# Kernel tuning notes

Hardware: AMD Instinct MI355X
Metric: run time of the kernel (lower is better)

Reference implementation:

```python
import jax, jax.numpy as jnp
import numpy as np

N, E, F0, HEADS, B, OUT = 100000, 1600000, 128, 4, 64, 32
CHANNELS = [16, 8, 4, 2]
NEG_SLOPE = 0.2


def setup_inputs() -> dict:
    key = jax.random.key(0)
    ks = jax.random.split(key, 40)
    inp = {}
    inp['x'] = jax.random.normal(ks[0], (N, F0), dtype=jnp.float32)
    inp['edge_index'] = jax.random.randint(ks[1], (2, E), 0, N, dtype=jnp.int64)
    inp['batch'] = jnp.sort(jax.random.randint(ks[2], (N,), 0, B, dtype=jnp.int64))
    # GATConv params per layer: W [in, heads*out], att_src/att_dst [heads, out], bias [heads*out]
    in_dim = F0
    ki = 3
    for li, oc in enumerate(CHANNELS, start=1):
        scale = 1.0 / np.sqrt(in_dim)
        inp[f'W{li}'] = jax.random.normal(ks[ki], (in_dim, HEADS * oc), dtype=jnp.float32) * scale
        inp[f'a_src{li}'] = jax.random.normal(ks[ki + 1], (HEADS, oc), dtype=jnp.float32) * 0.1
        inp[f'a_dst{li}'] = jax.random.normal(ks[ki + 2], (HEADS, oc), dtype=jnp.float32) * 0.1
        inp[f'b{li}'] = jnp.zeros((HEADS * oc,), dtype=jnp.float32)
        ki += 3
        in_dim = HEADS * oc
    inp['W_fc'] = jax.random.normal(ks[ki], (2 * HEADS, OUT), dtype=jnp.float32) * (1.0 / np.sqrt(2 * HEADS))
    inp['b_fc'] = jnp.zeros((OUT,), dtype=jnp.float32)
    return inp


def gat_layer(x, src, dst, W, a_src, a_dst, b, oc):
    n = x.shape[0]
    h = (x @ W).reshape(n, HEADS, oc)                    # [N, H, C]
    al_s = jnp.einsum('nhc,hc->nh', h, a_src)            # [N, H]
    al_d = jnp.einsum('nhc,hc->nh', h, a_dst)
    e = jax.nn.leaky_relu(al_s[src] + al_d[dst], NEG_SLOPE)  # [E, H]
    # segment softmax over incoming edges per destination node
    m = jax.ops.segment_max(e, dst, num_segments=n)
    m = jnp.where(jnp.isfinite(m), m, 0.0)
    ex = jnp.exp(e - m[dst])
    s = jax.ops.segment_sum(ex, dst, num_segments=n)
    alpha = ex / (s[dst] + 1e-16)                        # [E, H]
    out = jax.ops.segment_sum(h[src] * alpha[:, :, None], dst, num_segments=n)
    return out.reshape(n, HEADS * oc) + b


def reference(x, edge_index, batch, W1, a_src1, a_dst1, b1, W2, a_src2, a_dst2, b2,
              W3, a_src3, a_dst3, b3, W4, a_src4, a_dst4, b4, W_fc, b_fc):
    n = x.shape[0]
    loops = jnp.arange(n, dtype=edge_index.dtype)
    src = jnp.concatenate([edge_index[0], loops])   # PyG GATConv adds self-loops
    dst = jnp.concatenate([edge_index[1], loops])
    params = [(W1, a_src1, a_dst1, b1), (W2, a_src2, a_dst2, b2),
              (W3, a_src3, a_dst3, b3), (W4, a_src4, a_dst4, b4)]
    h = x
    for (W, a_s, a_d, b), oc in zip(params, CHANNELS):
        h = jax.nn.relu(gat_layer(h, src, dst, W, a_s, a_d, b, oc))
        # dropout(0.3) is identity at inference
    # global mean pool over graphs in the batch
    sums = jax.ops.segment_sum(h, batch, num_segments=B)
    cnt = jax.ops.segment_sum(jnp.ones((n,), h.dtype), batch, num_segments=B)
    pooled = sums / jnp.maximum(cnt, 1.0)[:, None]
    return pooled @ W_fc + b_fc
```

## Files before the change

kernel.cpp:

```cpp
#include <hip/hip_runtime.h>
#include <hip/hip_bf16.h>

#define NNODES 100000
#define NEDGES 1600000
#define NHEADS 4
#define NGRAPH 64
#define NOUTF  32
#define BSH    9
#define NBUK   ((NNODES + 511) >> 9)
#define BPAD   16
#define BCAP   9216
#define CGRID  512
#define G1GRID ((NNODES + 63) / 64)

__device__ __forceinline__ unsigned short f2bf(float f) {
    union { float f; unsigned u; } v;
    v.f = f;
    unsigned r = v.u + 0x7FFF + ((v.u >> 16) & 1);
    return (unsigned short)(r >> 16);
}
__device__ __forceinline__ float bflo(unsigned u) {
    union { unsigned u; float f; } v;
    v.u = u << 16;
    return v.f;
}
__device__ __forceinline__ float bfhi(unsigned u) {
    union { unsigned u; float f; } v;
    v.u = u & 0xFFFF0000u;
    return v.f;
}

__device__ __forceinline__ bool ei_is_int64(const int* __restrict__ ei) {
    int acc = 0;
    #pragma unroll
    for (int i = 0; i < 32; i++) acc |= ei[2 * i + 1];
    return acc == 0;
}

__device__ __forceinline__ void fma4(float4& a, float s, const float4& b) {
    a.x += s * b.x;
    a.y += s * b.y;
    a.z += s * b.z;
    a.w += s * b.w;
}

__global__ __launch_bounds__(256) void gat_coarse_gemm1_kernel(
        const int* __restrict__ ei, const int* __restrict__ bt,
        int* __restrict__ bkcur, int* __restrict__ packed, int* __restrict__ bat,
        const float* __restrict__ x, const float* __restrict__ W1,
        const float* __restrict__ as1, const float* __restrict__ ad1,
        unsigned short* __restrict__ h1, float* __restrict__ al_s,
        float* __restrict__ al_d, int ne, int n) {
    __shared__ float smem[64 * 64 + 64 * 132];
    const int tid = threadIdx.x;
    if (blockIdx.x < CGRID) {
        int* hist = (int*)smem;
        int* base = hist + NBUK;
        for (int i = tid; i < NBUK; i += 256) hist[i] = 0;
        __syncthreads();
        bool wide = ei_is_int64(ei);
        int chunk = (ne + CGRID - 1) / CGRID;
        int e0 = blockIdx.x * chunk;
        int e1 = min(e0 + chunk, ne);
        for (int i = e0 + tid; i < e1; i += 256) {
            int d = wide ? ei[2 * (ne + i)] : ei[ne + i];
            atomicAdd(&hist[d >> BSH], 1);
        }
        __syncthreads();
        for (int i = tid; i < NBUK; i += 256)
            base[i] = hist[i] ? atomicAdd(&bkcur[i * BPAD], hist[i]) : 0;
        __syncthreads();
        for (int i = tid; i < NBUK; i += 256) hist[i] = 0;
        __syncthreads();
        for (int i = e0 + tid; i < e1; i += 256) {
            int s = wide ? ei[2 * i] : ei[i];
            int d = wide ? ei[2 * (ne + i)] : ei[ne + i];
            int bk = d >> BSH;
            int pos = base[bk] + atomicAdd(&hist[bk], 1);
            if (pos < BCAP) packed[bk * BCAP + pos] = s | ((d & 511) << 17);
        }
        int gid = blockIdx.x * 256 + tid;
        for (int i = gid; i < n; i += CGRID * 256) bat[i] = wide ? bt[2 * i] : bt[i];
    } else {
        constexpr int DIN = 128, DOUT = 64, KTILE = 64;
        constexpr int OG = DOUT / 4;
        constexpr int NPB = 64;
        constexpr int S = DIN + 4;
        constexpr int C = DOUT / NHEADS;
        float* Wl = smem;
        float* xs = smem + KTILE * DOUT;
        const int base = (blockIdx.x - CGRID) * NPB;
        constexpr int KC = DIN / 4;
        for (int i = tid; i < NPB * KC; i += 256) {
            int nn = i / KC, kc = i - nn * KC;
            int nd = base + nn;
            float4 v = (nd < n) ? ((const float4*)x)[(size_t)nd * KC + kc]
                                : make_float4(0.f, 0.f, 0.f, 0.f);
            *(float4*)&xs[nn * S + kc * 4] = v;
        }
        const int og = tid % OG;
        const int ng = tid / OG;
        const int n0 = ng * 4;
        float4 acc[4] = {};
        for (int kt = 0; kt < DIN; kt += KTILE) {
            __syncthreads();
            for (int i = tid; i < KTILE * OG; i += 256)
                ((float4*)Wl)[i] = ((const float4*)W1)[kt * OG + i];
            __syncthreads();
            #pragma unroll 2
            for (int k = 0; k < KTILE; k += 4) {
                float4 wv[4], xv[4];
                #pragma unroll
                for (int j = 0; j < 4; j++)
                    wv[j] = *(const float4*)&Wl[(k + j) * DOUT + og * 4];
                #pragma unroll
                for (int r = 0; r < 4; r++)
                    xv[r] = *(const float4*)&xs[(n0 + r) * S + kt + k];
                #pragma unroll
                for (int r = 0; r < 4; r++) {
                    fma4(acc[r], xv[r].x, wv[0]);
                    fma4(acc[r], xv[r].y, wv[1]);
                    fma4(acc[r], xv[r].z, wv[2]);
                    fma4(acc[r], xv[r].w, wv[3]);
                }
            }
        }
        float4 asv = ((const float4*)as1)[og];
        float4 adv = ((const float4*)ad1)[og];
        #pragma unroll
        for (int r = 0; r < 4; r++) {
            int node = base + n0 + r;
            bool ok = node < n;
            if (ok) {
                ushort4 o;
                o.x = f2bf(acc[r].x);
                o.y = f2bf(acc[r].y);
                o.z = f2bf(acc[r].z);
                o.w = f2bf(acc[r].w);
                ((ushort4*)h1)[(size_t)node * OG + og] = o;
            }
            float ps = acc[r].x * asv.x + acc[r].y * asv.y + acc[r].z * asv.z + acc[r].w * asv.w;
            float pd = acc[r].x * adv.x + acc[r].y * adv.y + acc[r].z * adv.z + acc[r].w * adv.w;
            #pragma unroll
            for (int off = 1; off < C / 4; off <<= 1) {
                ps += __shfl_xor(ps, off);
                pd += __shfl_xor(pd, off);
            }
            if (ok && (og % (C / 4)) == 0) {
                int hh = og / (C / 4);
                al_s[node * NHEADS + hh] = ps;
                al_d[node * NHEADS + hh] = pd;
            }
        }
    }
}

__global__ __launch_bounds__(1024) void gat_fine_kernel(
        const int* __restrict__ packed, const int* __restrict__ bkcur,
        int* __restrict__ row_ptr, int* __restrict__ col, int n) {
    __shared__ int bscan[256];
    __shared__ int dg[512];
    __shared__ int excl[512];
    __shared__ int partial[256];
    __shared__ int cur[512];
    int b = blockIdx.x;
    int tid = threadIdx.x;
    if (tid < 256) bscan[tid] = (tid < NBUK) ? bkcur[tid * BPAD] : 0;
    if (tid < 512) dg[tid] = 0;
    __syncthreads();
    for (int off = 1; off < 256; off <<= 1) {
        int u = (tid < 256 && tid >= off) ? bscan[tid - off] : 0;
        __syncthreads();
        if (tid < 256) bscan[tid] += u;
        __syncthreads();
    }
    int cntb = bkcur[b * BPAD];
    int csr0 = bscan[b] - cntb;
    int pbeg = b * BCAP;
    int pend = pbeg + cntb;
    for (int t = pbeg + tid; t < pend; t += 1024)
        atomicAdd(&dg[packed[t] >> 17], 1);
    __syncthreads();
    int a0 = 0, a1 = 0, s = 0;
    if (tid < 256) {
        a0 = dg[2 * tid];
        a1 = dg[2 * tid + 1];
        s = a0 + a1;
        partial[tid] = s;
    }
    __syncthreads();
    for (int off = 1; off < 256; off <<= 1) {
        int u = (tid < 256 && tid >= off) ? partial[tid - off] : 0;
        __syncthreads();
        if (tid < 256) partial[tid] += u;
        __syncthreads();
    }
    if (tid < 256) {
        int ebase = partial[tid] - s;
        excl[2 * tid] = ebase;
        excl[2 * tid + 1] = ebase + a0;
        cur[2 * tid] = ebase;
        cur[2 * tid + 1] = ebase + a0;
    }
    __syncthreads();
    int node0 = b << BSH;
    if (tid < 512) {
        int nd = node0 + tid;
        if (nd < n) row_ptr[nd] = csr0 + excl[tid];
    }
    if (b == NBUK - 1 && tid == 0) row_ptr[n] = bscan[NBUK - 1];
    for (int t = pbeg + tid; t < pend; t += 1024) {
        int v = packed[t];
        int pos = atomicAdd(&cur[v >> 17], 1);
        col[csr0 + pos] = v & 0x1FFFF;
    }
}

template<int DIN, int DOUT, int KTILE, bool BF16OUT>
__global__ __launch_bounds__(256) void gat_gemm_attn_kernel(
        const float* __restrict__ in, const float* __restrict__ W,
        const float* __restrict__ a_src, const float* __restrict__ a_dst,
        void* __restrict__ hout, float* __restrict__ al_s, float* __restrict__ al_d, int n) {
    constexpr int OG = DOUT / 4;
    constexpr int NPB = 1024 / OG;
    constexpr int S = DIN + 4;
    constexpr int C = DOUT / NHEADS;
    __shared__ float Wl[KTILE * DOUT];
    __shared__ float xs[NPB * S];
    const int tid = threadIdx.x;
    const int base = blockIdx.x * NPB;
    constexpr int KC = DIN / 4;
    for (int i = tid; i < NPB * KC; i += 256) {
        int nn = i / KC, kc = i - nn * KC;
        int nd = base + nn;
        float4 v = (nd < n) ? ((const float4*)in)[(size_t)nd * KC + kc]
                            : make_float4(0.f, 0.f, 0.f, 0.f);
        *(float4*)&xs[nn * S + kc * 4] = v;
    }
    const int og = tid % OG;
    const int ng = tid / OG;
    const int n0 = ng * 4;
    float4 acc[4] = {};
    for (int kt = 0; kt < DIN; kt += KTILE) {
        __syncthreads();
        for (int i = tid; i < KTILE * OG; i += 256)
            ((float4*)Wl)[i] = ((const float4*)W)[kt * OG + i];
        __syncthreads();
        #pragma unroll 2
        for (int k = 0; k < KTILE; k += 4) {
            float4 wv[4], xv[4];
            #pragma unroll
            for (int j = 0; j < 4; j++)
                wv[j] = *(const float4*)&Wl[(k + j) * DOUT + og * 4];
            #pragma unroll
            for (int r = 0; r < 4; r++)
                xv[r] = *(const float4*)&xs[(n0 + r) * S + kt + k];
            #pragma unroll
            for (int r = 0; r < 4; r++) {
                fma4(acc[r], xv[r].x, wv[0]);
                fma4(acc[r], xv[r].y, wv[1]);
                fma4(acc[r], xv[r].z, wv[2]);
                fma4(acc[r], xv[r].w, wv[3]);
            }
        }
    }
    float4 asv = ((const float4*)a_src)[og];
    float4 adv = ((const float4*)a_dst)[og];
    #pragma unroll
    for (int r = 0; r < 4; r++) {
        int node = base + n0 + r;
        bool ok = node < n;
        if (ok) {
            if constexpr (BF16OUT) {
                ushort4 o;
                o.x = f2bf(acc[r].x);
                o.y = f2bf(acc[r].y);
                o.z = f2bf(acc[r].z);
                o.w = f2bf(acc[r].w);
                ((ushort4*)hout)[(size_t)node * OG + og] = o;
            } else {
                ((float4*)hout)[(size_t)node * OG + og] = acc[r];
            }
        }
        if constexpr (C >= 4) {
            float ps = acc[r].x * asv.x + acc[r].y * asv.y + acc[r].z * asv.z + acc[r].w * asv.w;
            float pd = acc[r].x * adv.x + acc[r].y * adv.y + acc[r].z * adv.z + acc[r].w * adv.w;
            #pragma unroll
            for (int off = 1; off < C / 4; off <<= 1) {
                ps += __shfl_xor(ps, off);
                pd += __shfl_xor(pd, off);
            }
            if (ok && (og % (C / 4)) == 0) {
                int hh = og / (C / 4);
                al_s[node * NHEADS + hh] = ps;
                al_d[node * NHEADS + hh] = pd;
            }
        } else {
            if (ok) {
                al_s[node * NHEADS + 2 * og]     = acc[r].x * asv.x + acc[r].y * asv.y;
                al_s[node * NHEADS + 2 * og + 1] = acc[r].z * asv.z + acc[r].w * asv.w;
                al_d[node * NHEADS + 2 * og]     = acc[r].x * adv.x + acc[r].y * adv.y;
                al_d[node * NHEADS + 2 * og + 1] = acc[r].z * adv.z + acc[r].w * adv.w;
            }
        }
    }
}

template<int G>
__global__ __launch_bounds__(256) void gat_agg_group_kernel(
        const unsigned short* __restrict__ h, const float* __restrict__ al_s,
        const float* __restrict__ al_d, const int* __restrict__ row_ptr,
        const int* __restrict__ col, const float* __restrict__ bias,
        float* __restrict__ out, int n) {
    constexpr int L = G / 8;
    constexpr int PW = 64 / L;
    constexpr int C = G / NHEADS;
    int lane = threadIdx.x & 63;
    int sub = lane & (L - 1);
    int gidx = lane / L;
    int node = blockIdx.x * (4 * PW) + (threadIdx.x >> 6) * PW + gidx;
    if (node >= n) return;
    int beg = row_ptr[node];
    int cnt = row_ptr[node + 1] - beg;
    const uint4* h4 = (const uint4*)h;
    float acc[8] = {};
    int j0 = sub * 8;
    if constexpr (C >= 8) {
        const int hh = (sub * 8) / C;
        float ald = al_d[node * NHEADS + hh];
        float ws = 0.f;
        int total = cnt + 1;
        int t = 0;
        for (; t + 2 <= total; t += 2) {
            int s0 = col[beg + t];
            int s1 = (t + 1 < cnt) ? col[beg + t + 1] : node;
            float e0 = al_s[s0 * NHEADS + hh] + ald;
            float e1 = al_s[s1 * NHEADS + hh] + ald;
            uint4 hv0 = h4[(size_t)s0 * L + sub];
            uint4 hv1 = h4[(size_t)s1 * L + sub];
            e0 = (e0 > 0.f) ? e0 : 0.2f * e0;
            e1 = (e1 > 0.f) ? e1 : 0.2f * e1;
            float w0 = __expf(e0);
            float w1 = __expf(e1);
            ws += w0;
            acc[0] += w0 * bflo(hv0.x);
            acc[1] += w0 * bfhi(hv0.x);
            acc[2] += w0 * bflo(hv0.y);
            acc[3] += w0 * bfhi(hv0.y);
            acc[4] += w0 * bflo(hv0.z);
            acc[5] += w0 * bfhi(hv0.z);
            acc[6] += w0 * bflo(hv0.w);
            acc[7] += w0 * bfhi(hv0.w);
            ws += w1;
            acc[0] += w1 * bflo(hv1.x);
            acc[1] += w1 * bfhi(hv1.x);
            acc[2] += w1 * bflo(hv1.y);
            acc[3] += w1 * bfhi(hv1.y);
            acc[4] += w1 * bflo(hv1.z);
            acc[5] += w1 * bfhi(hv1.z);
            acc[6] += w1 * bflo(hv1.w);
            acc[7] += w1 * bfhi(hv1.w);
        }
        if (t < total) {
            int s0 = (t < cnt) ? col[beg + t] : node;
            float e0 = al_s[s0 * NHEADS + hh] + ald;
            uint4 hv0 = h4[(size_t)s0 * L + sub];
            e0 = (e0 > 0.f) ? e0 : 0.2f * e0;
            float w0 = __expf(e0);
            ws += w0;
            acc[0] += w0 * bflo(hv0.x);
            acc[1] += w0 * bfhi(hv0.x);
            acc[2] += w0 * bflo(hv0.y);
            acc[3] += w0 * bfhi(hv0.y);
            acc[4] += w0 * bflo(hv0.z);
            acc[5] += w0 * bfhi(hv0.z);
            acc[6] += w0 * bflo(hv0.w);
            acc[7] += w0 * bfhi(hv0.w);
        }
        float inv = 1.f / (ws + 1e-16f);
        #pragma unroll
        for (int k = 0; k < 8; k++) acc[k] = acc[k] * inv + bias[j0 + k];
    } else {
        const int hh0 = 2 * sub, hh1 = 2 * sub + 1;
        float ald0 = al_d[node * NHEADS + hh0];
        float ald1 = al_d[node * NHEADS + hh1];
        float ws0 = 0.f, ws1 = 0.f;
        int total = cnt + 1;
        int t = 0;
        for (; t + 2 <= total; t += 2) {
            int s0 = col[beg + t];
            int s1 = (t + 1 < cnt) ? col[beg + t + 1] : node;
            float e00 = al_s[s0 * NHEADS + hh0] + ald0;
            float e01 = al_s[s0 * NHEADS + hh1] + ald1;
            float e10 = al_s[s1 * NHEADS + hh0] + ald0;
            float e11 = al_s[s1 * NHEADS + hh1] + ald1;
            uint4 hv0 = h4[(size_t)s0 * L + sub];
            uint4 hv1 = h4[(size_t)s1 * L + sub];
            e00 = (e00 > 0.f) ? e00 : 0.2f * e00;
            e01 = (e01 > 0.f) ? e01 : 0.2f * e01;
            e10 = (e10 > 0.f) ? e10 : 0.2f * e10;
            e11 = (e11 > 0.f) ? e11 : 0.2f * e11;
            float w00 = __expf(e00);
            float w01 = __expf(e01);
            float w10 = __expf(e10);
            float w11 = __expf(e11);
            ws0 += w00;
            ws1 += w01;
            acc[0] += w00 * bflo(hv0.x);
            acc[1] += w00 * bfhi(hv0.x);
            acc[2] += w00 * bflo(hv0.y);
            acc[3] += w00 * bfhi(hv0.y);
            acc[4] += w01 * bflo(hv0.z);
            acc[5] += w01 * bfhi(hv0.z);
            acc[6] += w01 * bflo(hv0.w);
            acc[7] += w01 * bfhi(hv0.w);
            ws0 += w10;
            ws1 += w11;
            acc[0] += w10 * bflo(hv1.x);
            acc[1] += w10 * bfhi(hv1.x);
            acc[2] += w10 * bflo(hv1.y);
            acc[3] += w10 * bfhi(hv1.y);
            acc[4] += w11 * bflo(hv1.z);
            acc[5] += w11 * bfhi(hv1.z);
            acc[6] += w11 * bflo(hv1.w);
            acc[7] += w11 * bfhi(hv1.w);
        }
        if (t < total) {
            int s0 = (t < cnt) ? col[beg + t] : node;
            float e00 = al_s[s0 * NHEADS + hh0] + ald0;
            float e01 = al_s[s0 * NHEADS + hh1] + ald1;
            uint4 hv0 = h4[(size_t)s0 * L + sub];
            e00 = (e00 > 0.f) ? e00 : 0.2f * e00;
            e01 = (e01 > 0.f) ? e01 : 0.2f * e01;
            float w00 = __expf(e00);
            float w01 = __expf(e01);
            ws0 += w00;
            ws1 += w01;
            acc[0] += w00 * bflo(hv0.x);
            acc[1] += w00 * bfhi(hv0.x);
            acc[2] += w00 * bflo(hv0.y);
            acc[3] += w00 * bfhi(hv0.y);
            acc[4] += w01 * bflo(hv0.z);
            acc[5] += w01 * bfhi(hv0.z);
            acc[6] += w01 * bflo(hv0.w);
            acc[7] += w01 * bfhi(hv0.w);
        }
        float inv0 = 1.f / (ws0 + 1e-16f);
        float inv1 = 1.f / (ws1 + 1e-16f);
        #pragma unroll
        for (int k = 0; k < 4; k++) acc[k] = acc[k] * inv0 + bias[j0 + k];
        #pragma unroll
        for (int k = 4; k < 8; k++) acc[k] = acc[k] * inv1 + bias[j0 + k];
    }
    float4 o0, o1;
    o0.x = (acc[0] > 0.f) ? acc[0] : 0.f;
    o0.y = (acc[1] > 0.f) ? acc[1] : 0.f;
    o0.z = (acc[2] > 0.f) ? acc[2] : 0.f;
    o0.w = (acc[3] > 0.f) ? acc[3] : 0.f;
    o1.x = (acc[4] > 0.f) ? acc[4] : 0.f;
    o1.y = (acc[5] > 0.f) ? acc[5] : 0.f;
    o1.z = (acc[6] > 0.f) ? acc[6] : 0.f;
    o1.w = (acc[7] > 0.f) ? acc[7] : 0.f;
    *(float4*)&out[(size_t)node * G + j0] = o0;
    *(float4*)&out[(size_t)node * G + j0 + 4] = o1;
}

__global__ __launch_bounds__(256) void gat_agg_f32_group_kernel(
        const float* __restrict__ h, const float* __restrict__ al_s, const float* __restrict__ al_d,
        const int* __restrict__ row_ptr, const int* __restrict__ col,
        const float* __restrict__ bias, float* __restrict__ out, int n) {
    constexpr int L = 2;
    constexpr int PW = 32;
    int lane = threadIdx.x & 63;
    int sub = lane & 1;
    int gidx = lane >> 1;
    int node = blockIdx.x * (4 * PW) + (threadIdx.x >> 6) * PW + gidx;
    if (node >= n) return;
    int beg = row_ptr[node];
    int cnt = row_ptr[node + 1] - beg;
    const int hh0 = 2 * sub, hh1 = 2 * sub + 1;
    float ald0 = al_d[node * NHEADS + hh0];
    float ald1 = al_d[node * NHEADS + hh1];
    const float4* h4 = (const float4*)h;
    float4 acc = make_float4(0.f, 0.f, 0.f, 0.f);
    float ws0 = 0.f, ws1 = 0.f;
    int total = cnt + 1;
    int t = 0;
    for (; t + 2 <= total; t += 2) {
        int s0 = col[beg + t];
        int s1 = (t + 1 < cnt) ? col[beg + t + 1] : node;
        float e00 = al_s[s0 * NHEADS + hh0] + ald0;
        float e01 = al_s[s0 * NHEADS + hh1] + ald1;
        float e10 = al_s[s1 * NHEADS + hh0] + ald0;
        float e11 = al_s[s1 * NHEADS + hh1] + ald1;
        float4 hv0 = h4[(size_t)s0 * L + sub];
        float4 hv1 = h4[(size_t)s1 * L + sub];
        e00 = (e00 > 0.f) ? e00 : 0.2f * e00;
        e01 = (e01 > 0.f) ? e01 : 0.2f * e01;
        e10 = (e10 > 0.f) ? e10 : 0.2f * e10;
        e11 = (e11 > 0.f) ? e11 : 0.2f * e11;
        float w00 = __expf(e00);
        float w01 = __expf(e01);
        float w10 = __expf(e10);
        float w11 = __expf(e11);
        ws0 += w00;
        ws1 += w01;
        acc.x += w00 * hv0.x;
        acc.y += w00 * hv0.y;
        acc.z += w01 * hv0.z;
        acc.w += w01 * hv0.w;
        ws0 += w10;
        ws1 += w11;
        acc.x += w10 * hv1.x;
        acc.y += w10 * hv1.y;
        acc.z += w11 * hv1.z;
        acc.w += w11 * hv1.w;
    }
    if (t < total) {
        int s0 = (t < cnt) ? col[beg + t] : node;
        float e00 = al_s[s0 * NHEADS + hh0] + ald0;
        float e01 = al_s[s0 * NHEADS + hh1] + ald1;
        float4 hv0 = h4[(size_t)s0 * L + sub];
        e00 = (e00 > 0.f) ? e00 : 0.2f * e00;
        e01 = (e01 > 0.f) ? e01 : 0.2f * e01;
        float w00 = __expf(e00);
        float w01 = __expf(e01);
        ws0 += w00;
        ws1 += w01;
        acc.x += w00 * hv0.x;
        acc.y += w00 * hv0.y;
        acc.z += w01 * hv0.z;
        acc.w += w01 * hv0.w;
    }
    float4 bv = ((const float4*)bias)[sub];
    float4 v;
    v.x = acc.x / (ws0 + 1e-16f) + bv.x;
    v.y = acc.y / (ws0 + 1e-16f) + bv.y;
    v.z = acc.z / (ws1 + 1e-16f) + bv.z;
    v.w = acc.w / (ws1 + 1e-16f) + bv.w;
    v.x = (v.x > 0.f) ? v.x : 0.f;
    v.y = (v.y > 0.f) ? v.y : 0.f;
    v.z = (v.z > 0.f) ? v.z : 0.f;
    v.w = (v.w > 0.f) ? v.w : 0.f;
    ((float4*)out)[(size_t)node * L + sub] = v;
}

__global__ __launch_bounds__(256) void gat_poolfc_kernel(
        const float* __restrict__ x, const int* __restrict__ bat,
        const float* __restrict__ Wfc, const float* __restrict__ bfc,
        float* __restrict__ out, int n) {
    __shared__ float sh[256][9];
    int b = blockIdx.x;
    int tid = threadIdx.x;
    int lo = 0, hi = n;
    while (lo < hi) { int mid = (lo + hi) >> 1; if (bat[mid] < b) lo = mid + 1; else hi = mid; }
    int i0 = lo;
    hi = n;
    while (lo < hi) { int mid = (lo + hi) >> 1; if (bat[mid] < b + 1) lo = mid + 1; else hi = mid; }
    int i1 = lo;
    float a[8] = {};
    for (int i = i0 + tid; i < i1; i += 256) {
        float4 v0 = ((const float4*)x)[(size_t)i * 2];
        float4 v1 = ((const float4*)x)[(size_t)i * 2 + 1];
        a[0] += v0.x; a[1] += v0.y; a[2] += v0.z; a[3] += v0.w;
        a[4] += v1.x; a[5] += v1.y; a[6] += v1.z; a[7] += v1.w;
    }
    #pragma unroll
    for (int k = 0; k < 8; k++) sh[tid][k] = a[k];
    __syncthreads();
    for (int off = 128; off >= 1; off >>= 1) {
        if (tid < off)
            #pragma unroll
            for (int k = 0; k < 8; k++) sh[tid][k] += sh[tid + off][k];
        __syncthreads();
    }
    if (tid < NOUTF) {
        float c = (float)(i1 - i0);
        if (c < 1.f) c = 1.f;
        float acc = bfc[tid];
        #pragma unroll
        for (int d = 0; d < 8; d++) acc += (sh[0][d] / c) * Wfc[d * NOUTF + tid];
        out[b * NOUTF + tid] = acc;
    }
}

extern "C" void kernel_launch(void* const* d_in, const int* in_sizes, int n_in,
                              void* d_out, int out_size, void* d_ws, size_t ws_size,
                              hipStream_t stream) {
    const float* x = (const float*)d_in[0];
    const int* ei = (const int*)d_in[1];
    const int* batch = (const int*)d_in[2];
    const float* W1 = (const float*)d_in[3];
    const float* as1 = (const float*)d_in[4];
    const float* ad1 = (const float*)d_in[5];
    const float* b1 = (const float*)d_in[6];
    const float* W2 = (const float*)d_in[7];
    const float* as2 = (const float*)d_in[8];
    const float* ad2 = (const float*)d_in[9];
    const float* b2 = (const float*)d_in[10];
    const float* W3 = (const float*)d_in[11];
    const float* as3 = (const float*)d_in[12];
    const float* ad3 = (const float*)d_in[13];
    const float* b3 = (const float*)d_in[14];
    const float* W4 = (const float*)d_in[15];
    const float* as4 = (const float*)d_in[16];
    const float* ad4 = (const float*)d_in[17];
    const float* b4 = (const float*)d_in[18];
    const float* Wfc = (const float*)d_in[19];
    const float* bfc = (const float*)d_in[20];

    const int n = NNODES, ne = NEDGES;

    char* p = (char*)d_ws;
    auto carve = [&](size_t bytes) {
        char* r = p;
        p += (bytes + 255) & ~(size_t)255;
        return r;
    };
    int* row_ptr = (int*)carve((size_t)(n + 1) * 4);
    int* col = (int*)carve((size_t)ne * 4);
    int* bkcur = (int*)carve(256 * BPAD * 4);
    int* packed = (int*)carve((size_t)NBUK * BCAP * 4);
    float* buf_h = (float*)carve((size_t)n * 64 * 4);
    float* buf_x = (float*)carve((size_t)n * 64 * 4);
    float* al_s = (float*)carve((size_t)n * NHEADS * 4);
    float* al_d = (float*)carve((size_t)n * NHEADS * 4);
    int* bat = (int*)carve((size_t)n * 4);
    unsigned short* h_bf16 = (unsigned short*)buf_h;

    hipMemsetAsync(bkcur, 0, 256 * BPAD * 4, stream);

    gat_coarse_gemm1_kernel<<<CGRID + G1GRID, 256, 0, stream>>>(
        ei, batch, bkcur, packed, bat, x, W1, as1, ad1, h_bf16, al_s, al_d, ne, n);

    gat_fine_kernel<<<NBUK, 1024, 0, stream>>>(packed, bkcur, row_ptr, col, n);

    gat_agg_group_kernel<64><<<(n + 31) / 32, 256, 0, stream>>>(
        h_bf16, al_s, al_d, row_ptr, col, b1, buf_x, n);

    gat_gemm_attn_kernel<64, 32, 64, true><<<(n + 127) / 128, 256, 0, stream>>>(
        buf_x, W2, as2, ad2, h_bf16, al_s, al_d, n);
    gat_agg_group_kernel<32><<<(n + 63) / 64, 256, 0, stream>>>(
        h_bf16, al_s, al_d, row_ptr, col, b2, buf_x, n);

    gat_gemm_attn_kernel<32, 16, 32, true><<<(n + 255) / 256, 256, 0, stream>>>(
        buf_x, W3, as3, ad3, h_bf16, al_s, al_d, n);
    gat_agg_group_kernel<16><<<(n + 127) / 128, 256, 0, stream>>>(
        h_bf16, al_s, al_d, row_ptr, col, b3, buf_x, n);

    gat_gemm_attn_kernel<16, 8, 16, false><<<(n + 511) / 512, 256, 0, stream>>>(
        buf_x, W4, as4, ad4, buf_h, al_s, al_d, n);
    gat_agg_f32_group_kernel<<<(n + 127) / 128, 256, 0, stream>>>(
        buf_h, al_s, al_d, row_ptr, col, b4, buf_x, n);

    gat_poolfc_kernel<<<NGRAPH, 256, 0, stream>>>(buf_x, bat, Wfc, bfc, (float*)d_out, n);
}
```

Before: 386.2 us.

## Interleave source attention scores with feature rows for layers two to four

Layers 2–4 now write each node's source attention scores into the same padded row as its projected features (16-byte header followed by the features, 96- or 64-byte stride). New aggregation kernels then read the score and the features for each neighbor from one row instead of two separate gathers. This targets the extra random memory transaction per edge. The cost is padded rows that use more bytes than the packed layout.

New measurement: 381.1 us. About the same (-1.3%).

```diff
diff --git a/kernel.cpp b/kernel.cpp
--- a/kernel.cpp
+++ b/kernel.cpp
@@ -216,11 +216,11 @@
     }
 }
 
-template<int DIN, int DOUT, int KTILE, bool BF16OUT>
+template<int DIN, int DOUT, int KTILE, bool BF16OUT, int STRIDE>
 __global__ __launch_bounds__(256) void gat_gemm_attn_kernel(
         const float* __restrict__ in, const float* __restrict__ W,
         const float* __restrict__ a_src, const float* __restrict__ a_dst,
-        void* __restrict__ hout, float* __restrict__ al_s, float* __restrict__ al_d, int n) {
+        char* __restrict__ hrow, float* __restrict__ al_d, int n) {
     constexpr int OG = DOUT / 4;
     constexpr int NPB = 1024 / OG;
     constexpr int S = DIN + 4;
@@ -270,6 +270,7 @@
     for (int r = 0; r < 4; r++) {
         int node = base + n0 + r;
         bool ok = node < n;
+        char* rp = hrow + (size_t)node * STRIDE;
         if (ok) {
             if constexpr (BF16OUT) {
                 ushort4 o;
@@ -277,9 +278,9 @@
                 o.y = f2bf(acc[r].y);
                 o.z = f2bf(acc[r].z);
                 o.w = f2bf(acc[r].w);
-                ((ushort4*)hout)[(size_t)node * OG + og] = o;
+                *(ushort4*)(rp + 16 + og * 8) = o;
             } else {
-                ((float4*)hout)[(size_t)node * OG + og] = acc[r];
+                *(float4*)(rp + 16 + og * 16) = acc[r];
             }
         }
         if constexpr (C >= 4) {
@@ -292,13 +293,13 @@
             }
             if (ok && (og % (C / 4)) == 0) {
                 int hh = og / (C / 4);
-                al_s[node * NHEADS + hh] = ps;
+                *(float*)(rp + 4 * hh) = ps;
                 al_d[node * NHEADS + hh] = pd;
             }
         } else {
             if (ok) {
-                al_s[node * NHEADS + 2 * og]     = acc[r].x * asv.x + acc[r].y * asv.y;
-                al_s[node * NHEADS + 2 * og + 1] = acc[r].z * asv.z + acc[r].w * asv.w;
+                *(float*)(rp + 8 * og)     = acc[r].x * asv.x + acc[r].y * asv.y;
+                *(float*)(rp + 8 * og + 4) = acc[r].z * asv.z + acc[r].w * asv.w;
                 al_d[node * NHEADS + 2 * og]     = acc[r].x * adv.x + acc[r].y * adv.y;
                 al_d[node * NHEADS + 2 * og + 1] = acc[r].z * adv.z + acc[r].w * adv.w;
             }
@@ -325,8 +326,92 @@
     const uint4* h4 = (const uint4*)h;
     float acc[8] = {};
     int j0 = sub * 8;
+    const int hh = (sub * 8) / C;
+    float ald = al_d[node * NHEADS + hh];
+    float ws = 0.f;
+    int total = cnt + 1;
+    int t = 0;
+    for (; t + 2 <= total; t += 2) {
+        int s0 = col[beg + t];
+        int s1 = (t + 1 < cnt) ? col[beg + t + 1] : node;
+        float e0 = al_s[s0 * NHEADS + hh] + ald;
+        float e1 = al_s[s1 * NHEADS + hh] + ald;
+        uint4 hv0 = h4[(size_t)s0 * L + sub];
+        uint4 hv1 = h4[(size_t)s1 * L + sub];
+        e0 = (e0 > 0.f) ? e0 : 0.2f * e0;
+        e1 = (e1 > 0.f) ? e1 : 0.2f * e1;
+        float w0 = __expf(e0);
+        float w1 = __expf(e1);
+        ws += w0;
+        acc[0] += w0 * bflo(hv0.x);
+        acc[1] += w0 * bfhi(hv0.x);
+        acc[2] += w0 * bflo(hv0.y);
+        acc[3] += w0 * bfhi(hv0.y);
+        acc[4] += w0 * bflo(hv0.z);
+        acc[5] += w0 * bfhi(hv0.z);
+        acc[6] += w0 * bflo(hv0.w);
+        acc[7] += w0 * bfhi(hv0.w);
+        ws += w1;
+        acc[0] += w1 * bflo(hv1.x);
+        acc[1] += w1 * bfhi(hv1.x);
+        acc[2] += w1 * bflo(hv1.y);
+        acc[3] += w1 * bfhi(hv1.y);
+        acc[4] += w1 * bflo(hv1.z);
+        acc[5] += w1 * bfhi(hv1.z);
+        acc[6] += w1 * bflo(hv1.w);
+        acc[7] += w1 * bfhi(hv1.w);
+    }
+    if (t < total) {
+        int s0 = (t < cnt) ? col[beg + t] : node;
+        float e0 = al_s[s0 * NHEADS + hh] + ald;
+        uint4 hv0 = h4[(size_t)s0 * L + sub];
+        e0 = (e0 > 0.f) ? e0 : 0.2f * e0;
+        float w0 = __expf(e0);
+        ws += w0;
+        acc[0] += w0 * bflo(hv0.x);
+        acc[1] += w0 * bfhi(hv0.x);
+        acc[2] += w0 * bflo(hv0.y);
+        acc[3] += w0 * bfhi(hv0.y);
+        acc[4] += w0 * bflo(hv0.z);
+        acc[5] += w0 * bfhi(hv0.z);
+        acc[6] += w0 * bflo(hv0.w);
+        acc[7] += w0 * bfhi(hv0.w);
+    }
+    float inv = 1.f / (ws + 1e-16f);
+    #pragma unroll
+    for (int k = 0; k < 8; k++) acc[k] = acc[k] * inv + bias[j0 + k];
+    float4 o0, o1;
+    o0.x = (acc[0] > 0.f) ? acc[0] : 0.f;
+    o0.y = (acc[1] > 0.f) ? acc[1] : 0.f;
+    o0.z = (acc[2] > 0.f) ? acc[2] : 0.f;
+    o0.w = (acc[3] > 0.f) ? acc[3] : 0.f;
+    o1.x = (acc[4] > 0.f) ? acc[4] : 0.f;
+    o1.y = (acc[5] > 0.f) ? acc[5] : 0.f;
+    o1.z = (acc[6] > 0.f) ? acc[6] : 0.f;
+    o1.w = (acc[7] > 0.f) ? acc[7] : 0.f;
+    *(float4*)&out[(size_t)node * G + j0] = o0;
+    *(float4*)&out[(size_t)node * G + j0 + 4] = o1;
+}
+
+template<int G, int STRIDE>
+__global__ __launch_bounds__(256) void gat_agg_row_kernel(
+        const char* __restrict__ hrow, const float* __restrict__ al_d,
+        const int* __restrict__ row_ptr, const int* __restrict__ col,
+        const float* __restrict__ bias, float* __restrict__ out, int n) {
+    constexpr int L = G / 8;
+    constexpr int PW = 64 / L;
+    constexpr int C = G / NHEADS;
+    int lane = threadIdx.x & 63;
+    int sub = lane & (L - 1);
+    int gidx = lane / L;
+    int node = blockIdx.x * (4 * PW) + (threadIdx.x >> 6) * PW + gidx;
+    if (node >= n) return;
+    int beg = row_ptr[node];
+    int cnt = row_ptr[node + 1] - beg;
+    float acc[8] = {};
+    int j0 = sub * 8;
     if constexpr (C >= 8) {
-        const int hh = (sub * 8) / C;
+        const int hh = sub;
         float ald = al_d[node * NHEADS + hh];
         float ws = 0.f;
         int total = cnt + 1;
@@ -334,10 +419,12 @@
         for (; t + 2 <= total; t += 2) {
             int s0 = col[beg + t];
             int s1 = (t + 1 < cnt) ? col[beg + t + 1] : node;
-            float e0 = al_s[s0 * NHEADS + hh] + ald;
-            float e1 = al_s[s1 * NHEADS + hh] + ald;
-            uint4 hv0 = h4[(size_t)s0 * L + sub];
-            uint4 hv1 = h4[(size_t)s1 * L + sub];
+            const char* r0 = hrow + (size_t)s0 * STRIDE;
+            const char* r1 = hrow + (size_t)s1 * STRIDE;
+            float e0 = *(const float*)(r0 + 4 * hh) + ald;
+            float e1 = *(const float*)(r1 + 4 * hh) + ald;
+            uint4 hv0 = *(const uint4*)(r0 + 16 + 16 * sub);
+            uint4 hv1 = *(const uint4*)(r1 + 16 + 16 * sub);
             e0 = (e0 > 0.f) ? e0 : 0.2f * e0;
             e1 = (e1 > 0.f) ? e1 : 0.2f * e1;
             float w0 = __expf(e0);
@@ -363,8 +450,9 @@
         }
         if (t < total) {
             int s0 = (t < cnt) ? col[beg + t] : node;
-            float e0 = al_s[s0 * NHEADS + hh] + ald;
-            uint4 hv0 = h4[(size_t)s0 * L + sub];
+            const char* r0 = hrow + (size_t)s0 * STRIDE;
+            float e0 = *(const float*)(r0 + 4 * hh) + ald;
+            uint4 hv0 = *(const uint4*)(r0 + 16 + 16 * sub);
             e0 = (e0 > 0.f) ? e0 : 0.2f * e0;
             float w0 = __expf(e0);
             ws += w0;
@@ -390,12 +478,16 @@
         for (; t + 2 <= total; t += 2) {
             int s0 = col[beg + t];
             int s1 = (t + 1 < cnt) ? col[beg + t + 1] : node;
-            float e00 = al_s[s0 * NHEADS + hh0] + ald0;
-            float e01 = al_s[s0 * NHEADS + hh1] + ald1;
-            float e10 = al_s[s1 * NHEADS + hh0] + ald0;
-            float e11 = al_s[s1 * NHEADS + hh1] + ald1;
-            uint4 hv0 = h4[(size_t)s0 * L + sub];
-            uint4 hv1 = h4[(size_t)s1 * L + sub];
+            const char* r0 = hrow + (size_t)s0 * STRIDE;
+            const char* r1 = hrow + (size_t)s1 * STRIDE;
+            float2 a0 = *(const float2*)(r0 + 8 * sub);
+            float2 a1 = *(const float2*)(r1 + 8 * sub);
+            uint4 hv0 = *(const uint4*)(r0 + 16 + 16 * sub);
+            uint4 hv1 = *(const uint4*)(r1 + 16 + 16 * sub);
+            float e00 = a0.x + ald0;
+            float e01 = a0.y + ald1;
+            float e10 = a1.x + ald0;
+            float e11 = a1.y + ald1;
             e00 = (e00 > 0.f) ? e00 : 0.2f * e00;
             e01 = (e01 > 0.f) ? e01 : 0.2f * e01;
             e10 = (e10 > 0.f) ? e10 : 0.2f * e10;
@@ -427,9 +519,11 @@
         }
         if (t < total) {
             int s0 = (t < cnt) ? col[beg + t] : node;
-            float e00 = al_s[s0 * NHEADS + hh0] + ald0;
-            float e01 = al_s[s0 * NHEADS + hh1] + ald1;
-            uint4 hv0 = h4[(size_t)s0 * L + sub];
+            const char* r0 = hrow + (size_t)s0 * STRIDE;
+            float2 a0 = *(const float2*)(r0 + 8 * sub);
+            uint4 hv0 = *(const uint4*)(r0 + 16 + 16 * sub);
+            float e00 = a0.x + ald0;
+            float e01 = a0.y + ald1;
             e00 = (e00 > 0.f) ? e00 : 0.2f * e00;
             e01 = (e01 > 0.f) ? e01 : 0.2f * e01;
             float w00 = __expf(e00);
@@ -465,8 +559,8 @@
     *(float4*)&out[(size_t)node * G + j0 + 4] = o1;
 }
 
-__global__ __launch_bounds__(256) void gat_agg_f32_group_kernel(
-        const float* __restrict__ h, const float* __restrict__ al_s, const float* __restrict__ al_d,
+__global__ __launch_bounds__(256) void gat_agg_f32row_kernel(
+        const char* __restrict__ hrow, const float* __restrict__ al_d,
         const int* __restrict__ row_ptr, const int* __restrict__ col,
         const float* __restrict__ bias, float* __restrict__ out, int n) {
     constexpr int L = 2;
@@ -481,7 +575,6 @@
     const int hh0 = 2 * sub, hh1 = 2 * sub + 1;
     float ald0 = al_d[node * NHEADS + hh0];
     float ald1 = al_d[node * NHEADS + hh1];
-    const float4* h4 = (const float4*)h;
     float4 acc = make_float4(0.f, 0.f, 0.f, 0.f);
     float ws0 = 0.f, ws1 = 0.f;
     int total = cnt + 1;
@@ -489,12 +582,16 @@
     for (; t + 2 <= total; t += 2) {
         int s0 = col[beg + t];
         int s1 = (t + 1 < cnt) ? col[beg + t + 1] : node;
-        float e00 = al_s[s0 * NHEADS + hh0] + ald0;
-        float e01 = al_s[s0 * NHEADS + hh1] + ald1;
-        float e10 = al_s[s1 * NHEADS + hh0] + ald0;
-        float e11 = al_s[s1 * NHEADS + hh1] + ald1;
-        float4 hv0 = h4[(size_t)s0 * L + sub];
-        float4 hv1 = h4[(size_t)s1 * L + sub];
+        const char* r0 = hrow + (size_t)s0 * 64;
+        const char* r1 = hrow + (size_t)s1 * 64;
+        float2 a0 = *(const float2*)(r0 + 8 * sub);
+        float2 a1 = *(const float2*)(r1 + 8 * sub);
+        float4 hv0 = *(const float4*)(r0 + 16 + 16 * sub);
+        float4 hv1 = *(const float4*)(r1 + 16 + 16 * sub);
+        float e00 = a0.x + ald0;
+        float e01 = a0.y + ald1;
+        float e10 = a1.x + ald0;
+        float e11 = a1.y + ald1;
         e00 = (e00 > 0.f) ? e00 : 0.2f * e00;
         e01 = (e01 > 0.f) ? e01 : 0.2f * e01;
         e10 = (e10 > 0.f) ? e10 : 0.2f * e10;
@@ -518,9 +615,11 @@
     }
     if (t < total) {
         int s0 = (t < cnt) ? col[beg + t] : node;
-        float e00 = al_s[s0 * NHEADS + hh0] + ald0;
-        float e01 = al_s[s0 * NHEADS + hh1] + ald1;
-        float4 hv0 = h4[(size_t)s0 * L + sub];
+        const char* r0 = hrow + (size_t)s0 * 64;
+        float2 a0 = *(const float2*)(r0 + 8 * sub);
+        float4 hv0 = *(const float4*)(r0 + 16 + 16 * sub);
+        float e00 = a0.x + ald0;
+        float e01 = a0.y + ald1;
         e00 = (e00 > 0.f) ? e00 : 0.2f * e00;
         e01 = (e01 > 0.f) ? e01 : 0.2f * e01;
         float w00 = __expf(e00);
@@ -627,6 +726,7 @@
     float* al_d = (float*)carve((size_t)n * NHEADS * 4);
     int* bat = (int*)carve((size_t)n * 4);
     unsigned short* h_bf16 = (unsigned short*)buf_h;
+    char* hrow = (char*)buf_h;
 
     hipMemsetAsync(bkcur, 0, 256 * BPAD * 4, stream);
 
@@ -638,20 +738,20 @@
     gat_agg_group_kernel<64><<<(n + 31) / 32, 256, 0, stream>>>(
         h_bf16, al_s, al_d, row_ptr, col, b1, buf_x, n);
 
-    gat_gemm_attn_kernel<64, 32, 64, true><<<(n + 127) / 128, 256, 0, stream>>>(
-        buf_x, W2, as2, ad2, h_bf16, al_s, al_d, n);
-    gat_agg_group_kernel<32><<<(n + 63) / 64, 256, 0, stream>>>(
-        h_bf16, al_s, al_d, row_ptr, col, b2, buf_x, n);
-
-    gat_gemm_attn_kernel<32, 16, 32, true><<<(n + 255) / 256, 256, 0, stream>>>(
-        buf_x, W3, as3, ad3, h_bf16, al_s, al_d, n);
-    gat_agg_group_kernel<16><<<(n + 127) / 128, 256, 0, stream>>>(
-        h_bf16, al_s, al_d, row_ptr, col, b3, buf_x, n);
-
-    gat_gemm_attn_kernel<16, 8, 16, false><<<(n + 511) / 512, 256, 0, stream>>>(
-        buf_x, W4, as4, ad4, buf_h, al_s, al_d, n);
-    gat_agg_f32_group_kernel<<<(n + 127) / 128, 256, 0, stream>>>(
-        buf_h, al_s, al_d, row_ptr, col, b4, buf_x, n);
+    gat_gemm_attn_kernel<64, 32, 64, true, 96><<<(n + 127) / 128, 256, 0, stream>>>(
+        buf_x, W2, as2, ad2, hrow, al_d, n);
+    gat_agg_row_kernel<32, 96><<<(n + 63) / 64, 256, 0, stream>>>(
+        hrow, al_d, row_ptr, col, b2, buf_x, n);
+
+    gat_gemm_attn_kernel<32, 16, 32, true, 64><<<(n + 255) / 256, 256, 0, stream>>>(
+        buf_x, W3, as3, ad3, hrow, al_d, n);
+    gat_agg_row_kernel<16, 64><<<(n + 127) / 128, 256, 0, stream>>>(
+        hrow, al_d, row_ptr, col, b3, buf_x, n);
+
+    gat_gemm_attn_kernel<16, 8, 16, false, 64><<<(n + 511) / 512, 256, 0, stream>>>(
+        buf_x, W4, as4, ad4, hrow, al_d, n);
+    gat_agg_f32row_kernel<<<(n + 127) / 128, 256, 0, stream>>>(
+        hrow, al_d, row_ptr, col, b4, buf_x, n);
 
     gat_poolfc_kernel<<<NGRAPH, 256, 0, stream>>>(buf_x, bat, Wfc, bfc, (float*)d_out, n);
 }
```
